# Kernel optimization log

Hardware: AMD Instinct MI355X
Metric: run time of the kernel (lower is better)

## Reference

```python
import jax, jax.numpy as jnp
import numpy as np

I, T, Q, K, E, H = 16, 64, 196, 32, 512, 8
D = E // H


def setup_inputs() -> dict:
    key = jax.random.key(0)
    ks = jax.random.split(key, 8)
    image = jax.random.normal(ks[0], (I, Q, E), dtype=jnp.float32)
    text = jax.random.normal(ks[1], (T, K, E), dtype=jnp.float32)
    text_mask = jax.random.randint(ks[2], (T, K), 0, 2).astype(bool)
    text_mask = text_mask.at[:, 0].set(True)  # avoid fully-masked rows
    s = 1.0 / np.sqrt(D)
    Wq = jax.random.normal(ks[3], (D, D), dtype=jnp.float32) * s
    Wk = jax.random.normal(ks[4], (D, D), dtype=jnp.float32) * s
    Wv = jax.random.normal(ks[5], (D, D), dtype=jnp.float32) * s
    Wo = jax.random.normal(ks[6], (E, E), dtype=jnp.float32) * (1.0 / np.sqrt(E))
    bo = jnp.zeros((E,), dtype=jnp.float32)
    return {"image": image, "text": text, "text_mask": text_mask,
            "Wq": Wq, "Wk": Wk, "Wv": Wv, "Wo": Wo, "bo": bo}


def reference(image, text, text_mask, Wq, Wk, Wv, Wo, bo):
    i, q_len, e = image.shape
    t, k_len, _ = text.shape
    img = image.reshape(i, q_len, H, D)   # i q h d
    txt = text.reshape(t, k_len, H, D)    # t k h d
    # torch Linear: x @ W.T (bias=False for q/k/v)
    query = jnp.einsum('iqhd,ed->iqhe', img, Wq)
    key_p = jnp.einsum('tkhd,ed->tkhe', txt, Wk)
    value = jnp.einsum('tkhd,ed->tkhe', txt, Wv)
    energy = jnp.einsum('tkhd,iqhd->ithqk', key_p, query)
    neg = jnp.finfo(jnp.float32).min
    energy = jnp.where(text_mask[None, :, None, None, :], energy, neg)
    scaled = energy / (e ** 0.5)
    attention = jax.nn.softmax(scaled, axis=-1)        # over k
    text_attention = jax.nn.softmax(scaled, axis=-2)   # over q
    out = jnp.einsum('ithqk,tkhd->itqhd', attention, value)
    out = out.reshape(i, t, q_len, e)                  # i t q (h d)
    out = jnp.einsum('itqe,fe->itqf', out, Wo) + bo    # fc_out
    out = out.mean(axis=2)                             # pooling_type='mean'
    return out, attention, text_attention
```

## Files before the change

### kernel.cpp

```cpp
#include <hip/hip_runtime.h>
#include <math.h>

#define I_N 16
#define T_N 64
#define Q_N 196
#define K_N 32
#define E_N 512
#define H_N 8
#define D_N 64

#define NEG_MASKED (-1.5038454e37f)
#define INV_SQRT_E (0.044194173824159216f)

typedef __attribute__((ext_vector_type(8))) short bf16x8;
typedef __attribute__((ext_vector_type(4))) float f32x4;

__device__ __forceinline__ short f2bf(float x) {
    unsigned u = __builtin_bit_cast(unsigned, x);
    unsigned r = (u + 0x7fffu + ((u >> 16) & 1u)) >> 16;
    return (short)r;
}
__device__ __forceinline__ float bf2f(short s) {
    unsigned u = ((unsigned)(unsigned short)s) << 16;
    return __builtin_bit_cast(float, u);
}
__device__ __forceinline__ void cvt8(float4 a, float4 b, bf16x8& hi, bf16x8& lo) {
    float xs[8] = {a.x, a.y, a.z, a.w, b.x, b.y, b.z, b.w};
#pragma unroll
    for (int j = 0; j < 8; ++j) {
        short h = f2bf(xs[j]);
        hi[j] = h;
        lo[j] = f2bf(xs[j] - bf2f(h));
    }
}

__global__ __launch_bounds__(512) void detect_mask_kernel(const unsigned int* __restrict__ mask,
                                                          int* __restrict__ flag) {
    __shared__ int notSimple, sawFloat;
    int tid = threadIdx.x;
    if (tid == 0) { notSimple = 0; sawFloat = 0; }
    __syncthreads();
    unsigned int v = mask[tid];
    if (v != 0u && v != 1u && v != 0x3f800000u) atomicOr(&notSimple, 1);
    if (v == 0x3f800000u) atomicOr(&sawFloat, 1);
    __syncthreads();
    if (tid == 0) flag[0] = notSimple ? 2 : (sawFloat ? 1 : 0);
}

__global__ __launch_bounds__(256) void proj_q_kernel(const float* __restrict__ x,
                                                     const float* __restrict__ W,
                                                     float* __restrict__ out) {
    __shared__ float sWt[64 * 65];
    __shared__ float sX[16 * 64];
    int tid = threadIdx.x;
    for (int j = tid; j < 4096; j += 256) {
        int n = j >> 6, d = j & 63;
        sWt[d * 65 + n] = W[j];
    }
    int rowBase = blockIdx.x * 16;
    for (int j = tid; j < 1024; j += 256) sX[j] = x[rowBase * 64 + j];
    __syncthreads();
    int wave = tid >> 6, lane = tid & 63;
    float acc[4] = {0.f, 0.f, 0.f, 0.f};
    for (int d = 0; d < 64; ++d) {
        float w = sWt[d * 65 + lane];
#pragma unroll
        for (int j = 0; j < 4; ++j) acc[j] += sX[(wave * 4 + j) * 64 + d] * w;
    }
#pragma unroll
    for (int j = 0; j < 4; ++j) {
        int r = rowBase + wave * 4 + j;
        int i = r / (Q_N * H_N);
        int rem = r - i * (Q_N * H_N);
        int q = rem >> 3, h = rem & 7;
        out[(((size_t)i * H_N + h) * Q_N + q) * 64 + lane] = acc[j];
    }
}

__global__ __launch_bounds__(256) void proj_kv_kernel(const float* __restrict__ x,
                                                      const float* __restrict__ Wk,
                                                      const float* __restrict__ Wv,
                                                      float* __restrict__ kout,
                                                      float* __restrict__ vout) {
    __shared__ float sWkT[64 * 65];
    __shared__ float sWvT[64 * 65];
    __shared__ float sX[16 * 64];
    int tid = threadIdx.x;
    for (int j = tid; j < 4096; j += 256) {
        int n = j >> 6, d = j & 63;
        sWkT[d * 65 + n] = Wk[j];
        sWvT[d * 65 + n] = Wv[j];
    }
    int rowBase = blockIdx.x * 16;
    for (int j = tid; j < 1024; j += 256) sX[j] = x[rowBase * 64 + j];
    __syncthreads();
    int wave = tid >> 6, lane = tid & 63;
    float ak[4] = {0.f, 0.f, 0.f, 0.f};
    float av[4] = {0.f, 0.f, 0.f, 0.f};
    for (int d = 0; d < 64; ++d) {
        float wk = sWkT[d * 65 + lane];
        float wv = sWvT[d * 65 + lane];
#pragma unroll
        for (int j = 0; j < 4; ++j) {
            float xv = sX[(wave * 4 + j) * 64 + d];
            ak[j] += xv * wk;
            av[j] += xv * wv;
        }
    }
#pragma unroll
    for (int j = 0; j < 4; ++j) {
        int r = rowBase + wave * 4 + j;
        int t = r >> 8;
        int rem = r & 255;
        int k = rem >> 3, h = rem & 7;
        size_t dst = (((size_t)t * H_N + h) * K_N + k) * 64 + lane;
        kout[dst] = ak[j];
        vout[dst] = av[j];
    }
}

__global__ __launch_bounds__(256) void transpose_wo_kernel(const float* __restrict__ Wo,
                                                           float* __restrict__ WoT) {
    __shared__ float tile[32][33];
    int tx = threadIdx.x & 31, ty = threadIdx.x >> 5;
    int e0 = blockIdx.x * 32, f0 = blockIdx.y * 32;
#pragma unroll
    for (int k = 0; k < 4; ++k) {
        int fy = ty + k * 8;
        tile[fy][tx] = Wo[(size_t)(f0 + fy) * E_N + e0 + tx];
    }
    __syncthreads();
#pragma unroll
    for (int k = 0; k < 4; ++k) {
        int ey = ty + k * 8;
        WoT[(size_t)(e0 + ey) * E_N + f0 + tx] = tile[tx][ey];
    }
}

__global__ __launch_bounds__(256) void attn_kernel(const float* __restrict__ qproj,
                                                   const float* __restrict__ kproj,
                                                   const float* __restrict__ vproj,
                                                   const int* __restrict__ mask,
                                                   const int* __restrict__ modeFlag,
                                                   float* __restrict__ attn_out,
                                                   float* __restrict__ tattn_out,
                                                   float* __restrict__ pooled) {
    __shared__ float sS[Q_N * 33];
    __shared__ float sMrow[Q_N];
    __shared__ float sRrow[Q_N];
    __shared__ float sColRed[8 * 32];
    __shared__ float sColRed2[8 * 32];
    __shared__ float sColMax[32];
    __shared__ float sColR[32];
    __shared__ float sCa[32];
    __shared__ float sMask[K_N];

    int tid = threadIdx.x;
    int bid = blockIdx.x;
    int h = bid & 7;
    int t = (bid >> 3) & 63;
    int i = bid >> 9;
    int lane = tid & 63, wave = tid >> 6;
    int quad = lane >> 4, lid = lane & 15;

    int mode = modeFlag[0];
    if (tid < K_N) {
        int idx = t * K_N + tid;
        bool keep;
        if (mode == 2)      keep = ((const unsigned char*)mask)[idx] != 0;
        else if (mode == 1) keep = ((const float*)mask)[idx] != 0.0f;
        else                keep = mask[idx] != 0;
        sMask[tid] = keep ? 1.0f : 0.0f;
    }
    __syncthreads();

    const float* kb = kproj + ((size_t)t * H_N + h) * (K_N * 64);
    bf16x8 Bh[2][2], Bl[2][2];
#pragma unroll
    for (int nt = 0; nt < 2; ++nt)
#pragma unroll
        for (int ks = 0; ks < 2; ++ks) {
            const float* p = kb + (nt * 16 + lid) * 64 + ks * 32 + quad * 8;
            cvt8(*(const float4*)p, *(const float4*)(p + 4), Bh[nt][ks], Bl[nt][ks]);
        }

    const float* qbh = qproj + ((size_t)i * H_N + h) * (Q_N * 64);
    float keep0 = sMask[lid], keep1 = sMask[16 + lid];

    for (int mt = wave; mt < 13; mt += 4) {
        int qbase = mt * 16;
        int qr = qbase + lid; if (qr > Q_N - 1) qr = Q_N - 1;
        const float* ab = qbh + (size_t)qr * 64 + quad * 8;
        bf16x8 Ah0, Al0, Ah1, Al1;
        cvt8(*(const float4*)ab, *(const float4*)(ab + 4), Ah0, Al0);
        cvt8(*(const float4*)(ab + 32), *(const float4*)(ab + 36), Ah1, Al1);

        f32x4 acc0 = {0.f, 0.f, 0.f, 0.f}, acc1 = {0.f, 0.f, 0.f, 0.f};
        acc0 = __builtin_amdgcn_mfma_f32_16x16x32_bf16(Al0, Bh[0][0], acc0, 0, 0, 0);
        acc0 = __builtin_amdgcn_mfma_f32_16x16x32_bf16(Ah0, Bl[0][0], acc0, 0, 0, 0);
        acc0 = __builtin_amdgcn_mfma_f32_16x16x32_bf16(Ah0, Bh[0][0], acc0, 0, 0, 0);
        acc0 = __builtin_amdgcn_mfma_f32_16x16x32_bf16(Al1, Bh[0][1], acc0, 0, 0, 0);
        acc0 = __builtin_amdgcn_mfma_f32_16x16x32_bf16(Ah1, Bl[0][1], acc0, 0, 0, 0);
        acc0 = __builtin_amdgcn_mfma_f32_16x16x32_bf16(Ah1, Bh[0][1], acc0, 0, 0, 0);
        acc1 = __builtin_amdgcn_mfma_f32_16x16x32_bf16(Al0, Bh[1][0], acc1, 0, 0, 0);
        acc1 = __builtin_amdgcn_mfma_f32_16x16x32_bf16(Ah0, Bl[1][0], acc1, 0, 0, 0);
        acc1 = __builtin_amdgcn_mfma_f32_16x16x32_bf16(Ah0, Bh[1][0], acc1, 0, 0, 0);
        acc1 = __builtin_amdgcn_mfma_f32_16x16x32_bf16(Al1, Bh[1][1], acc1, 0, 0, 0);
        acc1 = __builtin_amdgcn_mfma_f32_16x16x32_bf16(Ah1, Bl[1][1], acc1, 0, 0, 0);
        acc1 = __builtin_amdgcn_mfma_f32_16x16x32_bf16(Ah1, Bh[1][1], acc1, 0, 0, 0);

        float mrow[4], rrow[4];
#pragma unroll
        for (int reg = 0; reg < 4; ++reg) {
            float s0 = keep0 != 0.f ? acc0[reg] * INV_SQRT_E : NEG_MASKED;
            float s1 = keep1 != 0.f ? acc1[reg] * INV_SQRT_E : NEG_MASKED;
            float pm = fmaxf(s0, s1);
            pm = fmaxf(pm, __shfl_xor(pm, 1));
            pm = fmaxf(pm, __shfl_xor(pm, 2));
            pm = fmaxf(pm, __shfl_xor(pm, 4));
            pm = fmaxf(pm, __shfl_xor(pm, 8));
            float e0 = __expf(s0 - pm), e1 = __expf(s1 - pm);
            float ps = e0 + e1;
            ps += __shfl_xor(ps, 1);
            ps += __shfl_xor(ps, 2);
            ps += __shfl_xor(ps, 4);
            ps += __shfl_xor(ps, 8);
            float r = 1.0f / ps;
            mrow[reg] = pm; rrow[reg] = r;
            int q = qbase + quad * 4 + reg;
            if (q < Q_N) {
                float* arow = attn_out + (size_t)bid * (Q_N * K_N) + q * K_N;
                arow[lid] = e0 * r;
                arow[16 + lid] = e1 * r;
                sS[q * 33 + lid] = s0;
                sS[q * 33 + 16 + lid] = s1;
            }
        }
        if (lid == 0) {
#pragma unroll
            for (int reg = 0; reg < 4; ++reg) {
                int q = qbase + quad * 4 + reg;
                if (q < Q_N) { sMrow[q] = mrow[reg]; sRrow[q] = rrow[reg]; }
            }
        }
    }
    __syncthreads();

    int kc = tid & 31, sub = tid >> 5;
    {
        float m = -INFINITY;
        for (int qq = sub; qq < Q_N; qq += 8) m = fmaxf(m, sS[qq * 33 + kc]);
        sColRed[sub * 32 + kc] = m;
    }
    __syncthreads();
    if (tid < 32) {
        float mm = sColRed[tid];
#pragma unroll
        for (int s2 = 1; s2 < 8; ++s2) mm = fmaxf(mm, sColRed[s2 * 32 + tid]);
        sColMax[tid] = mm;
    }
    __syncthreads();
    {
        float mcol = sColMax[kc];
        float csum = 0.f, casum = 0.f;
        for (int qq = sub; qq < Q_N; qq += 8) {
            float v = sS[qq * 33 + kc];
            float e = __expf(v - mcol);
            sS[qq * 33 + kc] = e;
            csum += e;
            casum += __expf(v - sMrow[qq]) * sRrow[qq];
        }
        sColRed[sub * 32 + kc] = csum;
        sColRed2[sub * 32 + kc] = casum;
    }
    __syncthreads();
    if (tid < 32) {
        float s1 = 0.f, s2v = 0.f;
#pragma unroll
        for (int s2 = 0; s2 < 8; ++s2) {
            s1 += sColRed[s2 * 32 + tid];
            s2v += sColRed2[s2 * 32 + tid];
        }
        sColR[tid] = 1.0f / s1;
        sCa[tid] = s2v;
    }
    __syncthreads();

    {
        float* tbase = tattn_out + (size_t)bid * (Q_N * K_N);
        for (int j = tid; j < Q_N * K_N; j += 256) {
            int qq = j >> 5, k = j & 31;
            tbase[j] = sS[qq * 33 + k] * sColR[k];
        }
    }

    if (tid < 64) {
        const float* vb = vproj + ((size_t)t * H_N + h) * (K_N * 64) + tid;
        float acc = 0.f;
#pragma unroll
        for (int k = 0; k < K_N; ++k) acc += sCa[k] * vb[k * 64];
        pooled[((size_t)(i * T_N + t)) * E_N + h * 64 + tid] = acc;
    }
}

__global__ __launch_bounds__(256) void fc_out_kernel(const float* __restrict__ pooled,
                                                     const float* __restrict__ WoT,
                                                     const float* __restrict__ bo,
                                                     float* __restrict__ out) {
    __shared__ float sPT[E_N * 4];
    int tid = threadIdx.x;
    int p0 = blockIdx.x * 4;
#pragma unroll
    for (int j = 0; j < 4; ++j) {
        sPT[tid * 4 + j] = pooled[(size_t)(p0 + j) * E_N + tid];
        sPT[(256 + tid) * 4 + j] = pooled[(size_t)(p0 + j) * E_N + 256 + tid];
    }
    __syncthreads();
    const float4* sPT4 = (const float4*)sPT;
    int f = blockIdx.y * 256 + tid;
    float4 acc = make_float4(0.f, 0.f, 0.f, 0.f);
    for (int e = 0; e < E_N; e += 2) {
        float w0 = WoT[(size_t)e * E_N + f];
        float w1 = WoT[(size_t)(e + 1) * E_N + f];
        float4 pv0 = sPT4[e];
        float4 pv1 = sPT4[e + 1];
        acc.x += pv0.x * w0 + pv1.x * w1;
        acc.y += pv0.y * w0 + pv1.y * w1;
        acc.z += pv0.z * w0 + pv1.z * w1;
        acc.w += pv0.w * w0 + pv1.w * w1;
    }
    const float invQ = 1.0f / 196.0f;
    float b = bo[f];
    out[(size_t)(p0 + 0) * E_N + f] = b + acc.x * invQ;
    out[(size_t)(p0 + 1) * E_N + f] = b + acc.y * invQ;
    out[(size_t)(p0 + 2) * E_N + f] = b + acc.z * invQ;
    out[(size_t)(p0 + 3) * E_N + f] = b + acc.w * invQ;
}

extern "C" void kernel_launch(void* const* d_in, const int* in_sizes, int n_in,
                              void* d_out, int out_size, void* d_ws, size_t ws_size,
                              hipStream_t stream) {
    const float* image = (const float*)d_in[0];
    const float* text  = (const float*)d_in[1];
    const int*   mask  = (const int*)d_in[2];
    const float* Wq    = (const float*)d_in[3];
    const float* Wk    = (const float*)d_in[4];
    const float* Wv    = (const float*)d_in[5];
    const float* Wo    = (const float*)d_in[6];
    const float* bo    = (const float*)d_in[7];
    float* out = (float*)d_out;

    float* qproj  = (float*)d_ws;
    float* kproj  = qproj + (size_t)I_N * Q_N * H_N * D_N;
    float* vproj  = kproj + (size_t)T_N * K_N * H_N * D_N;
    float* pooled = vproj + (size_t)T_N * K_N * H_N * D_N;
    float* WoT    = pooled + (size_t)I_N * T_N * E_N;
    int*   mode   = (int*)(WoT + (size_t)E_N * E_N);

    float* attn  = out + (size_t)I_N * T_N * E_N;
    float* tattn = attn + (size_t)I_N * T_N * H_N * Q_N * K_N;

    detect_mask_kernel<<<1, 512, 0, stream>>>((const unsigned int*)mask, mode);
    proj_q_kernel<<<(I_N * Q_N * H_N) / 16, 256, 0, stream>>>(image, Wq, qproj);
    proj_kv_kernel<<<(T_N * K_N * H_N) / 16, 256, 0, stream>>>(text, Wk, Wv, kproj, vproj);
    transpose_wo_kernel<<<dim3(16, 16), 256, 0, stream>>>(Wo, WoT);
    attn_kernel<<<I_N * T_N * H_N, 256, 0, stream>>>(qproj, kproj, vproj, mask, mode,
                                                     attn, tattn, pooled);
    fc_out_kernel<<<dim3((I_N * T_N) / 4, 2), 256, 0, stream>>>(pooled, WoT, bo, out);
}
```

Before: 563.9 us.

## Precompute split-bf16 Q/K in projections and restructure attention softmax passes

The Q and K projection kernels now write pre-split bf16 hi/lo halves, with the 1/sqrt(E) scale folded into Q, so the attention kernel loads MFMA operands directly instead of converting fp32 per block. The attention kernel stores raw scores to shared memory, computes the column max during the MFMA loop and row stats in a separate pass. It then writes both attention and text-attention outputs in a single nontemporal store loop, instead of doing shuffle-based row softmax with scattered stores. This cuts conversion work and repeated Q reads, in exchange for extra exp evaluations in the final write loop and a slightly different rounding point for the scale.

```diff
diff --git a/kernel.cpp b/kernel.cpp
--- a/kernel.cpp
+++ b/kernel.cpp
@@ -24,15 +24,6 @@
     unsigned u = ((unsigned)(unsigned short)s) << 16;
     return __builtin_bit_cast(float, u);
 }
-__device__ __forceinline__ void cvt8(float4 a, float4 b, bf16x8& hi, bf16x8& lo) {
-    float xs[8] = {a.x, a.y, a.z, a.w, b.x, b.y, b.z, b.w};
-#pragma unroll
-    for (int j = 0; j < 8; ++j) {
-        short h = f2bf(xs[j]);
-        hi[j] = h;
-        lo[j] = f2bf(xs[j] - bf2f(h));
-    }
-}
 
 __global__ __launch_bounds__(512) void detect_mask_kernel(const unsigned int* __restrict__ mask,
                                                           int* __restrict__ flag) {
@@ -49,7 +40,8 @@
 
 __global__ __launch_bounds__(256) void proj_q_kernel(const float* __restrict__ x,
                                                      const float* __restrict__ W,
-                                                     float* __restrict__ out) {
+                                                     unsigned short* __restrict__ qh,
+                                                     unsigned short* __restrict__ ql) {
     __shared__ float sWt[64 * 65];
     __shared__ float sX[16 * 64];
     int tid = threadIdx.x;
@@ -73,14 +65,19 @@
         int i = r / (Q_N * H_N);
         int rem = r - i * (Q_N * H_N);
         int q = rem >> 3, h = rem & 7;
-        out[(((size_t)i * H_N + h) * Q_N + q) * 64 + lane] = acc[j];
+        size_t dst = (((size_t)i * H_N + h) * Q_N + q) * 64 + lane;
+        float a = acc[j] * INV_SQRT_E;
+        short hi = f2bf(a);
+        qh[dst] = (unsigned short)hi;
+        ql[dst] = (unsigned short)f2bf(a - bf2f(hi));
     }
 }
 
 __global__ __launch_bounds__(256) void proj_kv_kernel(const float* __restrict__ x,
                                                       const float* __restrict__ Wk,
                                                       const float* __restrict__ Wv,
-                                                      float* __restrict__ kout,
+                                                      unsigned short* __restrict__ kh,
+                                                      unsigned short* __restrict__ kl,
                                                       float* __restrict__ vout) {
     __shared__ float sWkT[64 * 65];
     __shared__ float sWvT[64 * 65];
@@ -114,7 +111,9 @@
         int rem = r & 255;
         int k = rem >> 3, h = rem & 7;
         size_t dst = (((size_t)t * H_N + h) * K_N + k) * 64 + lane;
-        kout[dst] = ak[j];
+        short hi = f2bf(ak[j]);
+        kh[dst] = (unsigned short)hi;
+        kl[dst] = (unsigned short)f2bf(ak[j] - bf2f(hi));
         vout[dst] = av[j];
     }
 }
@@ -137,8 +136,10 @@
     }
 }
 
-__global__ __launch_bounds__(256) void attn_kernel(const float* __restrict__ qproj,
-                                                   const float* __restrict__ kproj,
+__global__ __launch_bounds__(256) void attn_kernel(const unsigned short* __restrict__ qhi,
+                                                   const unsigned short* __restrict__ qlo,
+                                                   const unsigned short* __restrict__ khi,
+                                                   const unsigned short* __restrict__ klo,
                                                    const float* __restrict__ vproj,
                                                    const int* __restrict__ mask,
                                                    const int* __restrict__ modeFlag,
@@ -148,8 +149,9 @@
     __shared__ float sS[Q_N * 33];
     __shared__ float sMrow[Q_N];
     __shared__ float sRrow[Q_N];
-    __shared__ float sColRed[8 * 32];
+    __shared__ float sColRed[4 * 32];
     __shared__ float sColRed2[8 * 32];
+    __shared__ float sColRed3[8 * 32];
     __shared__ float sColMax[32];
     __shared__ float sColR[32];
     __shared__ float sCa[32];
@@ -174,26 +176,31 @@
     }
     __syncthreads();
 
-    const float* kb = kproj + ((size_t)t * H_N + h) * (K_N * 64);
+    size_t kbase = ((size_t)t * H_N + h) * (K_N * 64);
     bf16x8 Bh[2][2], Bl[2][2];
 #pragma unroll
     for (int nt = 0; nt < 2; ++nt)
 #pragma unroll
         for (int ks = 0; ks < 2; ++ks) {
-            const float* p = kb + (nt * 16 + lid) * 64 + ks * 32 + quad * 8;
-            cvt8(*(const float4*)p, *(const float4*)(p + 4), Bh[nt][ks], Bl[nt][ks]);
-        }
-
-    const float* qbh = qproj + ((size_t)i * H_N + h) * (Q_N * 64);
+            size_t off = kbase + (size_t)(nt * 16 + lid) * 64 + ks * 32 + quad * 8;
+            Bh[nt][ks] = *(const bf16x8*)(khi + off);
+            Bl[nt][ks] = *(const bf16x8*)(klo + off);
+        }
+
     float keep0 = sMask[lid], keep1 = sMask[16 + lid];
+    size_t qoff = ((size_t)i * H_N + h) * (Q_N * 64);
+
+    float cm0 = -INFINITY, cm1 = -INFINITY;
 
     for (int mt = wave; mt < 13; mt += 4) {
-        int qbase = mt * 16;
-        int qr = qbase + lid; if (qr > Q_N - 1) qr = Q_N - 1;
-        const float* ab = qbh + (size_t)qr * 64 + quad * 8;
-        bf16x8 Ah0, Al0, Ah1, Al1;
-        cvt8(*(const float4*)ab, *(const float4*)(ab + 4), Ah0, Al0);
-        cvt8(*(const float4*)(ab + 32), *(const float4*)(ab + 36), Ah1, Al1);
+        int qb = mt * 16;
+        int qr = qb + lid; if (qr > Q_N - 1) qr = Q_N - 1;
+        const unsigned short* ph = qhi + qoff + (size_t)qr * 64 + quad * 8;
+        const unsigned short* pl = qlo + qoff + (size_t)qr * 64 + quad * 8;
+        bf16x8 Ah0 = *(const bf16x8*)ph;
+        bf16x8 Ah1 = *(const bf16x8*)(ph + 32);
+        bf16x8 Al0 = *(const bf16x8*)pl;
+        bf16x8 Al1 = *(const bf16x8*)(pl + 32);
 
         f32x4 acc0 = {0.f, 0.f, 0.f, 0.f}, acc1 = {0.f, 0.f, 0.f, 0.f};
         acc0 = __builtin_amdgcn_mfma_f32_16x16x32_bf16(Al0, Bh[0][0], acc0, 0, 0, 0);
@@ -209,93 +216,93 @@
         acc1 = __builtin_amdgcn_mfma_f32_16x16x32_bf16(Ah1, Bl[1][1], acc1, 0, 0, 0);
         acc1 = __builtin_amdgcn_mfma_f32_16x16x32_bf16(Ah1, Bh[1][1], acc1, 0, 0, 0);
 
-        float mrow[4], rrow[4];
 #pragma unroll
         for (int reg = 0; reg < 4; ++reg) {
-            float s0 = keep0 != 0.f ? acc0[reg] * INV_SQRT_E : NEG_MASKED;
-            float s1 = keep1 != 0.f ? acc1[reg] * INV_SQRT_E : NEG_MASKED;
-            float pm = fmaxf(s0, s1);
-            pm = fmaxf(pm, __shfl_xor(pm, 1));
-            pm = fmaxf(pm, __shfl_xor(pm, 2));
-            pm = fmaxf(pm, __shfl_xor(pm, 4));
-            pm = fmaxf(pm, __shfl_xor(pm, 8));
-            float e0 = __expf(s0 - pm), e1 = __expf(s1 - pm);
-            float ps = e0 + e1;
-            ps += __shfl_xor(ps, 1);
-            ps += __shfl_xor(ps, 2);
-            ps += __shfl_xor(ps, 4);
-            ps += __shfl_xor(ps, 8);
-            float r = 1.0f / ps;
-            mrow[reg] = pm; rrow[reg] = r;
-            int q = qbase + quad * 4 + reg;
+            int q = qb + quad * 4 + reg;
             if (q < Q_N) {
-                float* arow = attn_out + (size_t)bid * (Q_N * K_N) + q * K_N;
-                arow[lid] = e0 * r;
-                arow[16 + lid] = e1 * r;
+                float s0 = keep0 != 0.f ? acc0[reg] : NEG_MASKED;
+                float s1 = keep1 != 0.f ? acc1[reg] : NEG_MASKED;
                 sS[q * 33 + lid] = s0;
                 sS[q * 33 + 16 + lid] = s1;
+                cm0 = fmaxf(cm0, s0);
+                cm1 = fmaxf(cm1, s1);
             }
         }
-        if (lid == 0) {
-#pragma unroll
-            for (int reg = 0; reg < 4; ++reg) {
-                int q = qbase + quad * 4 + reg;
-                if (q < Q_N) { sMrow[q] = mrow[reg]; sRrow[q] = rrow[reg]; }
-            }
-        }
+    }
+    cm0 = fmaxf(cm0, __shfl_xor(cm0, 16));
+    cm0 = fmaxf(cm0, __shfl_xor(cm0, 32));
+    cm1 = fmaxf(cm1, __shfl_xor(cm1, 16));
+    cm1 = fmaxf(cm1, __shfl_xor(cm1, 32));
+    if (lane < 16) {
+        sColRed[wave * 32 + lid] = cm0;
+        sColRed[wave * 32 + 16 + lid] = cm1;
+    }
+    __syncthreads();
+
+    if (tid < 32) {
+        float m = fmaxf(fmaxf(sColRed[tid], sColRed[32 + tid]),
+                        fmaxf(sColRed[64 + tid], sColRed[96 + tid]));
+        sColMax[tid] = m;
+    }
+    if (tid < Q_N) {
+        const float* r = &sS[tid * 33];
+        float rv[32];
+#pragma unroll
+        for (int k = 0; k < 32; ++k) rv[k] = r[k];
+#pragma unroll
+        for (int k = 0; k < 16; ++k) rv[k] = fmaxf(rv[k], rv[k + 16]);
+#pragma unroll
+        for (int k = 0; k < 8; ++k) rv[k] = fmaxf(rv[k], rv[k + 8]);
+        float m = fmaxf(fmaxf(fmaxf(rv[0], rv[1]), fmaxf(rv[2], rv[3])),
+                        fmaxf(fmaxf(rv[4], rv[5]), fmaxf(rv[6], rv[7])));
+        float s = 0.f;
+#pragma unroll
+        for (int k = 0; k < 32; ++k) s += __expf(r[k] - m);
+        sMrow[tid] = m;
+        sRrow[tid] = 1.0f / s;
     }
     __syncthreads();
 
     int kc = tid & 31, sub = tid >> 5;
     {
-        float m = -INFINITY;
-        for (int qq = sub; qq < Q_N; qq += 8) m = fmaxf(m, sS[qq * 33 + kc]);
-        sColRed[sub * 32 + kc] = m;
-    }
-    __syncthreads();
-    if (tid < 32) {
-        float mm = sColRed[tid];
-#pragma unroll
-        for (int s2 = 1; s2 < 8; ++s2) mm = fmaxf(mm, sColRed[s2 * 32 + tid]);
-        sColMax[tid] = mm;
-    }
-    __syncthreads();
-    {
         float mcol = sColMax[kc];
-        float csum = 0.f, casum = 0.f;
+        float cs = 0.f, ca = 0.f;
         for (int qq = sub; qq < Q_N; qq += 8) {
             float v = sS[qq * 33 + kc];
-            float e = __expf(v - mcol);
-            sS[qq * 33 + kc] = e;
-            csum += e;
-            casum += __expf(v - sMrow[qq]) * sRrow[qq];
-        }
-        sColRed[sub * 32 + kc] = csum;
-        sColRed2[sub * 32 + kc] = casum;
+            cs += __expf(v - mcol);
+            ca += __expf(v - sMrow[qq]) * sRrow[qq];
+        }
+        sColRed2[sub * 32 + kc] = cs;
+        sColRed3[sub * 32 + kc] = ca;
     }
     __syncthreads();
     if (tid < 32) {
-        float s1 = 0.f, s2v = 0.f;
-#pragma unroll
-        for (int s2 = 0; s2 < 8; ++s2) {
-            s1 += sColRed[s2 * 32 + tid];
-            s2v += sColRed2[s2 * 32 + tid];
+        float s1 = 0.f, s2 = 0.f;
+#pragma unroll
+        for (int s = 0; s < 8; ++s) {
+            s1 += sColRed2[s * 32 + tid];
+            s2 += sColRed3[s * 32 + tid];
         }
         sColR[tid] = 1.0f / s1;
-        sCa[tid] = s2v;
+        sCa[tid] = s2;
     }
     __syncthreads();
 
     {
-        float* tbase = tattn_out + (size_t)bid * (Q_N * K_N);
+        float* ab = attn_out + (size_t)bid * (Q_N * K_N);
+        float* tb = tattn_out + (size_t)bid * (Q_N * K_N);
         for (int j = tid; j < Q_N * K_N; j += 256) {
             int qq = j >> 5, k = j & 31;
-            tbase[j] = sS[qq * 33 + k] * sColR[k];
+            float v = sS[qq * 33 + k];
+            float a = __expf(v - sMrow[qq]) * sRrow[qq];
+            float ta = __expf(v - sColMax[k]) * sColR[k];
+            __builtin_nontemporal_store(a, ab + j);
+            __builtin_nontemporal_store(ta, tb + j);
         }
     }
 
     if (tid < 64) {
-        const float* vb = vproj + ((size_t)t * H_N + h) * (K_N * 64) + tid;
+        const float* vb = vproj + kbase + tid;
         float acc = 0.f;
 #pragma unroll
         for (int k = 0; k < K_N; ++k) acc += sCa[k] * vb[k * 64];
@@ -350,9 +357,11 @@
     const float* bo    = (const float*)d_in[7];
     float* out = (float*)d_out;
 
-    float* qproj  = (float*)d_ws;
-    float* kproj  = qproj + (size_t)I_N * Q_N * H_N * D_N;
-    float* vproj  = kproj + (size_t)T_N * K_N * H_N * D_N;
+    unsigned short* qhi = (unsigned short*)d_ws;
+    unsigned short* qlo = qhi + (size_t)I_N * Q_N * H_N * D_N;
+    unsigned short* khi = qlo + (size_t)I_N * Q_N * H_N * D_N;
+    unsigned short* klo = khi + (size_t)T_N * K_N * H_N * D_N;
+    float* vproj  = (float*)(klo + (size_t)T_N * K_N * H_N * D_N);
     float* pooled = vproj + (size_t)T_N * K_N * H_N * D_N;
     float* WoT    = pooled + (size_t)I_N * T_N * E_N;
     int*   mode   = (int*)(WoT + (size_t)E_N * E_N);
@@ -361,10 +370,10 @@
     float* tattn = attn + (size_t)I_N * T_N * H_N * Q_N * K_N;
 
     detect_mask_kernel<<<1, 512, 0, stream>>>((const unsigned int*)mask, mode);
-    proj_q_kernel<<<(I_N * Q_N * H_N) / 16, 256, 0, stream>>>(image, Wq, qproj);
-    proj_kv_kernel<<<(T_N * K_N * H_N) / 16, 256, 0, stream>>>(text, Wk, Wv, kproj, vproj);
+    proj_q_kernel<<<(I_N * Q_N * H_N) / 16, 256, 0, stream>>>(image, Wq, qhi, qlo);
+    proj_kv_kernel<<<(T_N * K_N * H_N) / 16, 256, 0, stream>>>(text, Wk, Wv, khi, klo, vproj);
     transpose_wo_kernel<<<dim3(16, 16), 256, 0, stream>>>(Wo, WoT);
-    attn_kernel<<<I_N * T_N * H_N, 256, 0, stream>>>(qproj, kproj, vproj, mask, mode,
+    attn_kernel<<<I_N * T_N * H_N, 256, 0, stream>>>(qhi, qlo, khi, klo, vproj, mask, mode,
                                                      attn, tattn, pooled);
     fc_out_kernel<<<dim3((I_N * T_N) / 4, 2), 256, 0, stream>>>(pooled, WoT, bo, out);
 }
```

New measurement: 510.9 us. -9.4%, faster.
